# Performance work log

Measured on AMD Instinct MI355X. Metric: run time of the kernel, lower is better.

The kernel has to match this reference:

```python
import jax, jax.numpy as jnp
import numpy as np

N, E, D, H, G = 50000, 640000, 128, 128, 64
EPS = 1e-5


def gcn_conv(x, row, col, W, b, n):
    # PyG GCNConv: linear transform, symmetric deg^-1/2 normalization (self-loops
    # already appended to row/col), scatter-add aggregation, then bias.
    h = x @ W  # [N, H]
    ones = jnp.ones(row.shape[0], dtype=h.dtype)
    deg = jax.ops.segment_sum(ones, col, num_segments=n)
    dinv = jnp.where(deg > 0, jax.lax.rsqrt(deg), 0.0)
    norm = dinv[row] * dinv[col]                       # [E+N]
    msg = h[row] * norm[:, None]                       # gather + scale
    out = jax.ops.segment_sum(msg, col, num_segments=n)  # scatter-add
    return out + b


def graph_layernorm(x, w, b):
    # PyG LayerNorm(mode='graph') with batch=None: normalize over the whole tensor.
    mu = x.mean()
    xc = x - mu
    std = jnp.sqrt((xc * xc).mean())
    return xc / (std + EPS) * w + b


def setup_inputs() -> dict:
    key = jax.random.key(0)
    ks = jax.random.split(key, 12)
    x = jax.random.normal(ks[0], (N, D), dtype=jnp.float32)
    edge_index = jax.random.randint(ks[1], (2, E), 0, N, dtype=jnp.int64)
    batch = jnp.sort(jax.random.randint(ks[2], (N,), 0, G, dtype=jnp.int64))
    s1 = 1.0 / np.sqrt(D)
    s2 = 1.0 / np.sqrt(H)
    return {
        "x": x,
        "edge_index": edge_index,
        "batch": batch,
        "W1": jax.random.normal(ks[3], (D, H), dtype=jnp.float32) * s1,
        "b1": jnp.zeros((H,), dtype=jnp.float32),
        "ln1_w": jnp.ones((H,), dtype=jnp.float32),
        "ln1_b": jnp.zeros((H,), dtype=jnp.float32),
        "W2": jax.random.normal(ks[4], (H, H), dtype=jnp.float32) * s2,
        "b2": jnp.zeros((H,), dtype=jnp.float32),
        "ln2_w": jnp.ones((H,), dtype=jnp.float32),
        "ln2_b": jnp.zeros((H,), dtype=jnp.float32),
        "fc_w": jax.random.normal(ks[5], (H, 1), dtype=jnp.float32) * s2,
        "fc_b": jnp.zeros((1,), dtype=jnp.float32),
    }


def reference(x, edge_index, batch, W1, b1, ln1_w, ln1_b, W2, b2, ln2_w, ln2_b, fc_w, fc_b):
    n = x.shape[0]
    loops = jnp.arange(n, dtype=edge_index.dtype)
    row = jnp.concatenate([edge_index[0], loops])  # add self-loops
    col = jnp.concatenate([edge_index[1], loops])

    h = gcn_conv(x, row, col, W1, b1, n)
    h = jax.nn.relu(graph_layernorm(h, ln1_w, ln1_b))
    h = gcn_conv(h, row, col, W2, b2, n)
    h = jax.nn.relu(graph_layernorm(h, ln2_w, ln2_b))

    # global_mean_pool over batch segment ids
    sums = jax.ops.segment_sum(h, batch, num_segments=G)          # [G, H]
    cnt = jax.ops.segment_sum(jnp.ones((n,), h.dtype), batch, num_segments=G)
    pooled = sums / jnp.maximum(cnt, 1.0)[:, None]

    logits = pooled @ fc_w + fc_b                                  # [G, 1]
    return jax.nn.sigmoid(logits).squeeze(-1)                      # [G]
```

## Files before the change

### kernel.cpp

```cpp
#include <hip/hip_runtime.h>
#include <math.h>

#define H 128
#define PC 8

typedef _Float16 half8v __attribute__((ext_vector_type(8)));
typedef float floatx4 __attribute__((ext_vector_type(4)));

__device__ __forceinline__ int lower_bound_i(const int* a, int n, int key) {
  int lo = 0, hi = n;
  while (lo < hi) { int mid = (lo + hi) >> 1; if (a[mid] < key) lo = mid + 1; else hi = mid; }
  return lo;
}

__global__ void k_initpack(const float* __restrict__ W1, const float* __restrict__ W2,
                           _Float16* __restrict__ PW1, _Float16* __restrict__ PW2,
                           int* cntE, float* slots, int n) {
  int b = blockIdx.x;
  int tid = threadIdx.x;
  if (b < 128) {
    int t = b * 256 + tid;
    const float* W = (t < 16384) ? W1 : W2;
    _Float16* PW = (t < 16384) ? PW1 : PW2;
    int u = t & 16383;
    int j = u & 7;
    int nn = (u >> 3) & 15;
    int quad = (u >> 7) & 3;
    int ks = (u >> 9) & 3;
    int ct = (u >> 11) & 7;
    PW[u] = (_Float16)W[(ks * 32 + quad * 8 + j) * H + ct * 16 + nn];
  } else {
    int i = (b - 128) * 256 + tid;
    int stride = 128 * 256;
    for (int j = i; j < n; j += stride) cntE[j] = 0;
    for (int j = i; j < 256; j += stride) slots[j] = 0.f;
  }
}

__global__ void k_count(const int* __restrict__ col, int* __restrict__ cntE,
                        int* __restrict__ perm, int E) {
  int e = blockIdx.x * blockDim.x + threadIdx.x;
  if (e < E) perm[e] = atomicAdd(&cntE[col[e]], 1);
}

__global__ void k_scan_block(const int* __restrict__ cnt, int* __restrict__ offs,
                             int* __restrict__ bsum, int n) {
  __shared__ int s[256];
  int tid = threadIdx.x;
  int i = blockIdx.x * 256 + tid;
  int v = (i < n) ? cnt[i] : 0;
  s[tid] = v;
  __syncthreads();
  for (int d = 1; d < 256; d <<= 1) {
    int t = (tid >= d) ? s[tid - d] : 0;
    __syncthreads();
    s[tid] += t;
    __syncthreads();
  }
  if (i < n) offs[i] = s[tid] - v;
  if (tid == 255) bsum[blockIdx.x] = s[255];
}

__global__ void k_scan_add(int* __restrict__ offs, const int* __restrict__ bsum,
                           const int* __restrict__ cntE, float* __restrict__ dinv, int n) {
  __shared__ int sh[4];
  int tid = threadIdx.x;
  int v = (tid < blockIdx.x) ? bsum[tid] : 0;
#pragma unroll
  for (int o = 32; o > 0; o >>= 1) v += __shfl_xor(v, o, 64);
  if ((tid & 63) == 0) sh[tid >> 6] = v;
  __syncthreads();
  int boff = sh[0] + sh[1] + sh[2] + sh[3];
  int i = blockIdx.x * 256 + tid;
  if (i < n) {
    offs[i] += boff;
    dinv[i] = rsqrtf((float)(cntE[i] + 1));
  }
}

__device__ __forceinline__ void gemm_tile_f32(const float* __restrict__ Xf,
                                              const _Float16* __restrict__ PW,
                                              const float* __restrict__ dinv,
                                              _Float16* __restrict__ O,
                                              int wave, int laneid, int n) {
  int m = laneid & 15;
  int quad = laneid >> 4;
  int r0 = wave * 16;
  int row = r0 + m;
  if (row >= n) row = n - 1;
  floatx4 acc[8] = {};
  const half8v* PB8 = (const half8v*)PW;
#pragma unroll
  for (int ks = 0; ks < 4; ks++) {
    int kb = ks * 32 + quad * 8;
    const float* xr = Xf + (size_t)row * H + kb;
    float4 u0 = *(const float4*)xr;
    float4 u1 = *(const float4*)(xr + 4);
    half8v a;
    a[0] = (_Float16)u0.x; a[1] = (_Float16)u0.y; a[2] = (_Float16)u0.z; a[3] = (_Float16)u0.w;
    a[4] = (_Float16)u1.x; a[5] = (_Float16)u1.y; a[6] = (_Float16)u1.z; a[7] = (_Float16)u1.w;
#pragma unroll
    for (int ct = 0; ct < 8; ct++) {
      half8v b = PB8[((ct * 4 + ks) * 4 + quad) * 16 + m];
      acc[ct] = __builtin_amdgcn_mfma_f32_16x16x32_f16(a, b, acc[ct], 0, 0, 0);
    }
  }
  float dv[4];
#pragma unroll
  for (int reg = 0; reg < 4; reg++) {
    int ro = r0 + quad * 4 + reg;
    dv[reg] = (ro < n) ? dinv[ro] : 0.f;
  }
#pragma unroll
  for (int ct = 0; ct < 8; ct++) {
#pragma unroll
    for (int reg = 0; reg < 4; reg++) {
      int ro = r0 + quad * 4 + reg;
      if (ro < n) O[(size_t)ro * H + ct * 16 + m] = (_Float16)(acc[ct][reg] * dv[reg]);
    }
  }
}

__global__ __launch_bounds__(256) void k_sg1(const int* __restrict__ row, const int* __restrict__ col,
                                             const int* __restrict__ offs, const int* __restrict__ perm,
                                             int* __restrict__ esrc, int E,
                                             const float* __restrict__ Xf,
                                             const _Float16* __restrict__ PW,
                                             const float* __restrict__ dinv,
                                             _Float16* __restrict__ O, int n, int GB) {
  int b = blockIdx.x;
  if (b < GB) {
    int wave = b * 4 + (threadIdx.x >> 6);
    int tiles = (n + 15) >> 4;
    if (wave >= tiles) return;
    gemm_tile_f32(Xf, PW, dinv, O, wave, threadIdx.x & 63, n);
  } else {
    int e = (b - GB) * 256 + threadIdx.x;
    if (e < E) {
      int c = col[e];
      esrc[offs[c] + perm[e]] = row[e];
    }
  }
}

__global__ __launch_bounds__(256) void k_gemm2(const _Float16* __restrict__ Xh,
                                               const _Float16* __restrict__ PW,
                                               const float* __restrict__ lnw,
                                               const float* __restrict__ lnb,
                                               const float* __restrict__ slot, float invM,
                                               const float* __restrict__ dinv,
                                               _Float16* __restrict__ O, int n) {
  int wave = blockIdx.x * 4 + (threadIdx.x >> 6);
  int tiles = (n + 15) >> 4;
  if (wave >= tiles) return;
  int lane = threadIdx.x & 63;
  int m = lane & 15;
  int quad = lane >> 4;
  int r0 = wave * 16;
  int row = r0 + m;
  if (row >= n) row = n - 1;

  float s = slot[lane], q = slot[64 + lane];
#pragma unroll
  for (int o = 32; o > 0; o >>= 1) { s += __shfl_xor(s, o, 64); q += __shfl_xor(q, o, 64); }
  float mu = s * invM;
  float var = fmaxf(q * invM - mu * mu, 0.f);
  float rs = 1.f / (sqrtf(var) + 1e-5f);

  floatx4 acc[8] = {};
  const half8v* PB8 = (const half8v*)PW;
#pragma unroll
  for (int ks = 0; ks < 4; ks++) {
    int kb = ks * 32 + quad * 8;
    half8v hv = *(const half8v*)(Xh + (size_t)row * H + kb);
    float4 w0 = *(const float4*)(lnw + kb);
    float4 w1 = *(const float4*)(lnw + kb + 4);
    float4 c0 = *(const float4*)(lnb + kb);
    float4 c1 = *(const float4*)(lnb + kb + 4);
    half8v a;
    a[0] = (_Float16)fmaxf(((float)hv[0] - mu) * rs * w0.x + c0.x, 0.f);
    a[1] = (_Float16)fmaxf(((float)hv[1] - mu) * rs * w0.y + c0.y, 0.f);
    a[2] = (_Float16)fmaxf(((float)hv[2] - mu) * rs * w0.z + c0.z, 0.f);
    a[3] = (_Float16)fmaxf(((float)hv[3] - mu) * rs * w0.w + c0.w, 0.f);
    a[4] = (_Float16)fmaxf(((float)hv[4] - mu) * rs * w1.x + c1.x, 0.f);
    a[5] = (_Float16)fmaxf(((float)hv[5] - mu) * rs * w1.y + c1.y, 0.f);
    a[6] = (_Float16)fmaxf(((float)hv[6] - mu) * rs * w1.z + c1.z, 0.f);
    a[7] = (_Float16)fmaxf(((float)hv[7] - mu) * rs * w1.w + c1.w, 0.f);
#pragma unroll
    for (int ct = 0; ct < 8; ct++) {
      half8v b = PB8[((ct * 4 + ks) * 4 + quad) * 16 + m];
      acc[ct] = __builtin_amdgcn_mfma_f32_16x16x32_f16(a, b, acc[ct], 0, 0, 0);
    }
  }
  float dv[4];
#pragma unroll
  for (int reg = 0; reg < 4; reg++) {
    int ro = r0 + quad * 4 + reg;
    dv[reg] = (ro < n) ? dinv[ro] : 0.f;
  }
#pragma unroll
  for (int ct = 0; ct < 8; ct++) {
#pragma unroll
    for (int reg = 0; reg < 4; reg++) {
      int ro = r0 + quad * 4 + reg;
      if (ro < n) O[(size_t)ro * H + ct * 16 + m] = (_Float16)(acc[ct][reg] * dv[reg]);
    }
  }
}

__global__ __launch_bounds__(256) void k_agg(const _Float16* __restrict__ Gs,
                                             _Float16* __restrict__ Out,
                                             const int* __restrict__ esrc, const int* __restrict__ offs,
                                             const int* __restrict__ cntE, const float* __restrict__ dinv,
                                             const float* __restrict__ bias, float* __restrict__ slot,
                                             int n) {
  int sub = threadIdx.x >> 4;
  int lane = threadIdx.x & 15;
  int i = blockIdx.x * 16 + sub;
  float sv = 0.f, sq = 0.f;
  if (i < n) {
    float di = dinv[i];
    half8v gself = *(const half8v*)&Gs[(size_t)i * H + 8 * lane];
    float acc[8];
#pragma unroll
    for (int e = 0; e < 8; e++) acc[e] = (float)gself[e];
    int beg = offs[i], cnt = cntE[i];
    for (int base = 0; base < cnt; base += 16) {
      int mm = cnt - base; if (mm > 16) mm = 16;
      int sid = 0;
      if (lane < mm) sid = esrc[beg + base + lane];
      int j = 0;
      for (; j + 8 <= mm; j += 8) {
        int sg[8]; half8v hg[8];
#pragma unroll
        for (int u = 0; u < 8; u++) sg[u] = __shfl(sid, j + u, 16);
#pragma unroll
        for (int u = 0; u < 8; u++) hg[u] = *(const half8v*)&Gs[(size_t)sg[u] * H + 8 * lane];
#pragma unroll
        for (int e = 0; e < 8; e++) {
          float t = 0.f;
#pragma unroll
          for (int u = 0; u < 8; u++) t += (float)hg[u][e];
          acc[e] += t;
        }
      }
      for (; j + 4 <= mm; j += 4) {
        int s0 = __shfl(sid, j + 0, 16);
        int s1 = __shfl(sid, j + 1, 16);
        int s2 = __shfl(sid, j + 2, 16);
        int s3 = __shfl(sid, j + 3, 16);
        half8v h0 = *(const half8v*)&Gs[(size_t)s0 * H + 8 * lane];
        half8v h1 = *(const half8v*)&Gs[(size_t)s1 * H + 8 * lane];
        half8v h2 = *(const half8v*)&Gs[(size_t)s2 * H + 8 * lane];
        half8v h3 = *(const half8v*)&Gs[(size_t)s3 * H + 8 * lane];
#pragma unroll
        for (int e = 0; e < 8; e++)
          acc[e] += (float)h0[e] + (float)h1[e] + (float)h2[e] + (float)h3[e];
      }
      for (; j < mm; j++) {
        int s = __shfl(sid, j, 16);
        half8v hv = *(const half8v*)&Gs[(size_t)s * H + 8 * lane];
#pragma unroll
        for (int e = 0; e < 8; e++) acc[e] += (float)hv[e];
      }
    }
    const float* bb = bias + 8 * lane;
    half8v vo;
#pragma unroll
    for (int e = 0; e < 8; e++) {
      float v = di * acc[e] + bb[e];
      vo[e] = (_Float16)v;
      sv += v;
      sq += v * v;
    }
    *(half8v*)&Out[(size_t)i * H + 8 * lane] = vo;
  }
#pragma unroll
  for (int o = 32; o > 0; o >>= 1) {
    sv += __shfl_xor(sv, o, 64);
    sq += __shfl_xor(sq, o, 64);
  }
  __shared__ float rsm[4], rqm[4];
  int wave = threadIdx.x >> 6;
  if ((threadIdx.x & 63) == 0) { rsm[wave] = sv; rqm[wave] = sq; }
  __syncthreads();
  if (threadIdx.x == 0) {
    float ts = rsm[0] + rsm[1] + rsm[2] + rsm[3];
    float tq = rqm[0] + rqm[1] + rqm[2] + rqm[3];
    int sl = blockIdx.x & 63;
    atomicAdd(&slot[sl], ts);
    atomicAdd(&slot[64 + sl], tq);
  }
}

__global__ __launch_bounds__(128) void k_pool(const _Float16* __restrict__ Hs,
                                              const int* __restrict__ batch,
                                              const float* __restrict__ lnw, const float* __restrict__ lnb,
                                              const float* __restrict__ slot, float invM,
                                              float* __restrict__ psum, int n) {
  int g = blockIdx.x / PC, q = blockIdx.x % PC;
  int t = threadIdx.x;
  int l = t & 63;
  float s = slot[l], qq = slot[64 + l];
#pragma unroll
  for (int o = 32; o > 0; o >>= 1) { s += __shfl_xor(s, o, 64); qq += __shfl_xor(qq, o, 64); }
  float mu = s * invM;
  float var = fmaxf(qq * invM - mu * mu, 0.f);
  float rs = 1.f / (sqrtf(var) + 1e-5f);

  int start = lower_bound_i(batch, n, g);
  int end = lower_bound_i(batch, n, g + 1);
  int tot = end - start;
  int per = (tot + PC - 1) / PC;
  int s0 = start + q * per;
  int e0 = s0 + per; if (e0 > end) e0 = end;
  float w = lnw[t], bb = lnb[t];
  float acc = 0.f;
  for (int i = s0; i < e0; i++) {
    float v = (float)Hs[(size_t)i * H + t];
    v = (v - mu) * rs * w + bb;
    acc += fmaxf(v, 0.f);
  }
  psum[(size_t)blockIdx.x * H + t] = acc;
}

__global__ __launch_bounds__(128) void k_fc(const float* __restrict__ psum, const int* __restrict__ batch,
                                            const float* __restrict__ fcw, const float* __restrict__ fcb,
                                            float* __restrict__ out, int n) {
  int g = blockIdx.x;
  int t = threadIdx.x;
  int start = lower_bound_i(batch, n, g);
  int end = lower_bound_i(batch, n, g + 1);
  float cnt = fmaxf((float)(end - start), 1.f);
  float tot = 0.f;
#pragma unroll
  for (int c = 0; c < PC; c++) tot += psum[(size_t)(g * PC + c) * H + t];
  float v = tot / cnt * fcw[t];
  int lane = t & 63, wave = t >> 6;
#pragma unroll
  for (int o = 32; o > 0; o >>= 1) v += __shfl_xor(v, o, 64);
  __shared__ float r2[2];
  if (lane == 0) r2[wave] = v;
  __syncthreads();
  if (t == 0) {
    float logit = r2[0] + r2[1] + fcb[0];
    out[g] = 1.f / (1.f + expf(-logit));
  }
}

extern "C" void kernel_launch(void* const* d_in, const int* in_sizes, int n_in,
                              void* d_out, int out_size, void* d_ws, size_t ws_size,
                              hipStream_t stream) {
  const float* x    = (const float*)d_in[0];
  const int*   ei   = (const int*)d_in[1];
  const int*   batch= (const int*)d_in[2];
  const float* W1   = (const float*)d_in[3];
  const float* b1   = (const float*)d_in[4];
  const float* ln1w = (const float*)d_in[5];
  const float* ln1b = (const float*)d_in[6];
  const float* W2   = (const float*)d_in[7];
  const float* b2   = (const float*)d_in[8];
  const float* ln2w = (const float*)d_in[9];
  const float* ln2b = (const float*)d_in[10];
  const float* fcw  = (const float*)d_in[11];
  const float* fcb  = (const float*)d_in[12];
  float* out = (float*)d_out;

  int N = in_sizes[2];
  int E = in_sizes[1] / 2;
  int G = out_size;

  char* p = (char*)d_ws;
  int*   cntE   = (int*)p;   p += (size_t)N * 4;
  int*   offs   = (int*)p;   p += (size_t)N * 4;
  float* dinv   = (float*)p; p += (size_t)N * 4;
  int*   perm   = (int*)p;   p += (size_t)E * 4;
  int*   esrc   = (int*)p;   p += (size_t)E * 4;
  _Float16* bufA = (_Float16*)p; p += (size_t)N * H * 2;
  _Float16* bufB = (_Float16*)p; p += (size_t)N * H * 2;
  _Float16* PW1  = (_Float16*)p; p += 16384 * 2;
  _Float16* PW2  = (_Float16*)p; p += 16384 * 2;
  float* slots  = (float*)p; p += 256 * 4;
  int*   bsum   = (int*)p;   p += 256 * 4;
  float* psum   = (float*)p; p += (size_t)G * PC * H * 4;

  const int* row = ei;
  const int* col = ei + E;

  k_initpack<<<256, 256, 0, stream>>>(W1, W2, PW1, PW2, cntE, slots, N);
  int EB = (E + 255) / 256;
  k_count<<<EB, 256, 0, stream>>>(col, cntE, perm, E);
  int NB = (N + 255) / 256;
  k_scan_block<<<NB, 256, 0, stream>>>(cntE, offs, bsum, N);
  k_scan_add<<<NB, 256, 0, stream>>>(offs, bsum, cntE, dinv, N);

  int tiles = (N + 15) / 16;
  int GB = (tiles + 3) / 4;
  float invM = 1.f / ((float)N * (float)H);

  k_sg1<<<GB + EB, 256, 0, stream>>>(row, col, offs, perm, esrc, E, x, PW1, dinv, bufA, N, GB);
  k_agg<<<(N + 15) / 16, 256, 0, stream>>>(bufA, bufB, esrc, offs, cntE, dinv, b1, slots, N);
  k_gemm2<<<GB, 256, 0, stream>>>(bufB, PW2, ln1w, ln1b, slots, invM, dinv, bufA, N);
  k_agg<<<(N + 15) / 16, 256, 0, stream>>>(bufA, bufB, esrc, offs, cntE, dinv, b2, slots + 128, N);
  k_pool<<<G * PC, 128, 0, stream>>>(bufB, batch, ln2w, ln2b, slots + 128, invM, psum, N);
  k_fc<<<G, 128, 0, stream>>>(psum, batch, fcw, fcb, out, N);
}
```

Measured before the change: 282.9 us.

## Pad CSR neighbor lists to multiples of 16 with zero-row sentinel

Each node's incoming-edge list in the CSR is padded to a multiple of 16 entries, and padding slots point to an extra zero row (index n) appended to the feature buffers. The aggregation kernel can then drop its 8/4/1 remainder loops and always issue 16 gathers per chunk, prefetching the next chunk's indices while the current one is summed. This gives more memory-level parallelism and fewer branches per chunk. The cost is extra gather traffic on the zero row, a larger esrc buffer that must be filled with the sentinel at init, and more registers per thread.

Measured after the change: 269.3 us. 4.8% less time.

```diff
diff --git a/kernel.cpp b/kernel.cpp
--- a/kernel.cpp
+++ b/kernel.cpp
@@ -15,7 +15,7 @@
 
 __global__ void k_initpack(const float* __restrict__ W1, const float* __restrict__ W2,
                            _Float16* __restrict__ PW1, _Float16* __restrict__ PW2,
-                           int* cntE, float* slots, int n) {
+                           int* cntE, float* slots, int* esrc, int cap, int n) {
   int b = blockIdx.x;
   int tid = threadIdx.x;
   if (b < 128) {
@@ -34,6 +34,7 @@
     int stride = 128 * 256;
     for (int j = i; j < n; j += stride) cntE[j] = 0;
     for (int j = i; j < 256; j += stride) slots[j] = 0.f;
+    for (int j = i; j < cap; j += stride) esrc[j] = n;
   }
 }
 
@@ -48,7 +49,7 @@
   __shared__ int s[256];
   int tid = threadIdx.x;
   int i = blockIdx.x * 256 + tid;
-  int v = (i < n) ? cnt[i] : 0;
+  int v = (i < n) ? ((cnt[i] + 15) & ~15) : 0;
   s[tid] = v;
   __syncthreads();
   for (int d = 1; d < 256; d <<= 1) {
@@ -130,6 +131,10 @@
                                              _Float16* __restrict__ O, int n, int GB) {
   int b = blockIdx.x;
   if (b < GB) {
+    if (b == 0 && threadIdx.x < 16) {
+      half8v z = {};
+      *(half8v*)&O[(size_t)n * H + threadIdx.x * 8] = z;
+    }
     int wave = b * 4 + (threadIdx.x >> 6);
     int tiles = (n + 15) >> 4;
     if (wave >= tiles) return;
@@ -150,6 +155,10 @@
                                                const float* __restrict__ slot, float invM,
                                                const float* __restrict__ dinv,
                                                _Float16* __restrict__ O, int n) {
+  if (blockIdx.x == 0 && threadIdx.x < 16) {
+    half8v z = {};
+    *(half8v*)&O[(size_t)n * H + threadIdx.x * 8] = z;
+  }
   int wave = blockIdx.x * 4 + (threadIdx.x >> 6);
   int tiles = (n + 15) >> 4;
   if (wave >= tiles) return;
@@ -224,44 +233,23 @@
     float acc[8];
 #pragma unroll
     for (int e = 0; e < 8; e++) acc[e] = (float)gself[e];
-    int beg = offs[i], cnt = cntE[i];
-    for (int base = 0; base < cnt; base += 16) {
-      int mm = cnt - base; if (mm > 16) mm = 16;
-      int sid = 0;
-      if (lane < mm) sid = esrc[beg + base + lane];
-      int j = 0;
-      for (; j + 8 <= mm; j += 8) {
-        int sg[8]; half8v hg[8];
-#pragma unroll
-        for (int u = 0; u < 8; u++) sg[u] = __shfl(sid, j + u, 16);
-#pragma unroll
-        for (int u = 0; u < 8; u++) hg[u] = *(const half8v*)&Gs[(size_t)sg[u] * H + 8 * lane];
-#pragma unroll
-        for (int e = 0; e < 8; e++) {
-          float t = 0.f;
-#pragma unroll
-          for (int u = 0; u < 8; u++) t += (float)hg[u][e];
-          acc[e] += t;
-        }
-      }
-      for (; j + 4 <= mm; j += 4) {
-        int s0 = __shfl(sid, j + 0, 16);
-        int s1 = __shfl(sid, j + 1, 16);
-        int s2 = __shfl(sid, j + 2, 16);
-        int s3 = __shfl(sid, j + 3, 16);
-        half8v h0 = *(const half8v*)&Gs[(size_t)s0 * H + 8 * lane];
-        half8v h1 = *(const half8v*)&Gs[(size_t)s1 * H + 8 * lane];
-        half8v h2 = *(const half8v*)&Gs[(size_t)s2 * H + 8 * lane];
-        half8v h3 = *(const half8v*)&Gs[(size_t)s3 * H + 8 * lane];
-#pragma unroll
-        for (int e = 0; e < 8; e++)
-          acc[e] += (float)h0[e] + (float)h1[e] + (float)h2[e] + (float)h3[e];
-      }
-      for (; j < mm; j++) {
-        int s = __shfl(sid, j, 16);
-        half8v hv = *(const half8v*)&Gs[(size_t)s * H + 8 * lane];
-#pragma unroll
-        for (int e = 0; e < 8; e++) acc[e] += (float)hv[e];
+    int beg = offs[i];
+    int c16 = (cntE[i] + 15) & ~15;
+    int sid = (c16 > 0) ? esrc[beg + lane] : 0;
+    for (int base = 0; base < c16; base += 16) {
+      int cur = sid;
+      if (base + 16 < c16) sid = esrc[beg + base + 16 + lane];
+      int sg[16]; half8v hg[16];
+#pragma unroll
+      for (int u = 0; u < 16; u++) sg[u] = __shfl(cur, u, 16);
+#pragma unroll
+      for (int u = 0; u < 16; u++) hg[u] = *(const half8v*)&Gs[(size_t)sg[u] * H + 8 * lane];
+#pragma unroll
+      for (int e = 0; e < 8; e++) {
+        float t0 = 0.f, t1 = 0.f;
+#pragma unroll
+        for (int u = 0; u < 8; u++) { t0 += (float)hg[u][e]; t1 += (float)hg[8 + u][e]; }
+        acc[e] += t0 + t1;
       }
     }
     const float* bb = bias + 8 * lane;
@@ -369,15 +357,16 @@
   int N = in_sizes[2];
   int E = in_sizes[1] / 2;
   int G = out_size;
+  int CAP = E + 15 * N;
 
   char* p = (char*)d_ws;
   int*   cntE   = (int*)p;   p += (size_t)N * 4;
   int*   offs   = (int*)p;   p += (size_t)N * 4;
   float* dinv   = (float*)p; p += (size_t)N * 4;
   int*   perm   = (int*)p;   p += (size_t)E * 4;
-  int*   esrc   = (int*)p;   p += (size_t)E * 4;
-  _Float16* bufA = (_Float16*)p; p += (size_t)N * H * 2;
-  _Float16* bufB = (_Float16*)p; p += (size_t)N * H * 2;
+  int*   esrc   = (int*)p;   p += (size_t)CAP * 4;
+  _Float16* bufA = (_Float16*)p; p += (size_t)(N + 1) * H * 2;
+  _Float16* bufB = (_Float16*)p; p += (size_t)(N + 1) * H * 2;
   _Float16* PW1  = (_Float16*)p; p += 16384 * 2;
   _Float16* PW2  = (_Float16*)p; p += 16384 * 2;
   float* slots  = (float*)p; p += 256 * 4;
@@ -387,7 +376,7 @@
   const int* row = ei;
   const int* col = ei + E;
 
-  k_initpack<<<256, 256, 0, stream>>>(W1, W2, PW1, PW2, cntE, slots, N);
+  k_initpack<<<256, 256, 0, stream>>>(W1, W2, PW1, PW2, cntE, slots, esrc, CAP, N);
   int EB = (E + 255) / 256;
   k_count<<<EB, 256, 0, stream>>>(col, cntE, perm, E);
   int NB = (N + 255) / 256;
```
